# Optimization experiments

Measured on AMD Instinct MI355X. Metric: run time of the kernel, lower is better.

Reference implementation:

```python
import jax, jax.numpy as jnp
import numpy as np
from jax import lax

B, N, D = 4, 2048, 1024
MAX_SEQ = 2048
GROUPS = 4  # math.gcd(1024, 4)
LN_EPS = 1e-5


def setup_inputs() -> dict:
    key = jax.random.key(0)
    ks = jax.random.split(key, 12)
    s = 0.02
    return {
        "x": jax.random.normal(ks[0], (B, N, D), jnp.float32),
        "Wq": jax.random.normal(ks[1], (D, D), jnp.float32) * s,
        "Wk": jax.random.normal(ks[2], (D, D), jnp.float32) * s,
        "Wv": jax.random.normal(ks[3], (D, D), jnp.float32) * s,
        "rel_bias": jax.random.normal(ks[4], (1, MAX_SEQ, MAX_SEQ), jnp.float32) * s,
        "conv_w": jax.random.normal(ks[5], (D, D // GROUPS, 3), jnp.float32) * s,
        "conv_b": jnp.zeros((D,), jnp.float32),
        "resg_w": jax.random.normal(ks[6], (D, D), jnp.float32) * s,
        "resg_b": jnp.zeros((D,), jnp.float32),
        "ln_g": jnp.ones((D,), jnp.float32),
        "ln_b": jnp.zeros((D,), jnp.float32),
        "fc1_w": jax.random.normal(ks[7], (D // 2, D), jnp.float32) * s,
        "fc1_b": jnp.zeros((D // 2,), jnp.float32),
        "fc2_w": jax.random.normal(ks[8], (1, D // 2), jnp.float32) * s,
        "fc2_b": jnp.zeros((1,), jnp.float32),
    }


def _forward(x, Wq, Wk, Wv, rel_bias, conv_w, conv_b, resg_w, resg_b,
             ln_g, ln_b, fc1_w, fc1_b, fc2_w, fc2_b):
    b, n, d = x.shape
    scale = 1.0 / jnp.sqrt(jnp.asarray(d, x.dtype))
    q = x @ Wq.T  # [b,n,dk]
    k = x @ Wk.T
    v = x @ Wv.T  # [b,n,dv]
    att = jnp.einsum("bqd,bkd->bqk", q, k) * scale + rel_bias[:, :n, :n]
    causal = jnp.tril(jnp.ones((n, n), bool))
    att = jnp.where(causal, att, jnp.asarray(-jnp.inf, att.dtype))
    att = jax.nn.softmax(att, axis=-1)  # dropout is identity at eval
    att_out = jnp.einsum("bqk,bkd->bqd", att, v)
    # grouped temporal conv over sequence dim: v [b,n,dv] -> NCH [b,dv,n]
    conv = lax.conv_general_dilated(
        v.transpose(0, 2, 1), conv_w, window_strides=(1,), padding=[(1, 1)],
        dimension_numbers=("NCH", "OIH", "NCH"), feature_group_count=GROUPS)
    conv = conv + conv_b[None, :, None]
    out = att_out + conv.transpose(0, 2, 1)
    res = jax.nn.sigmoid(out @ resg_w.T + resg_b)
    out = x + res * out
    mu = out.mean(-1, keepdims=True)
    var = out.var(-1, keepdims=True)
    out = (out - mu) * lax.rsqrt(var + LN_EPS) * ln_g + ln_b
    h = jax.nn.gelu(out @ fc1_w.T + fc1_b, approximate=False)
    return jax.nn.sigmoid(h @ fc2_w.T + fc2_b)


def reference(x, Wq, Wk, Wv, rel_bias, conv_w, conv_b, resg_w, resg_b,
              ln_g, ln_b, fc1_w, fc1_b, fc2_w, fc2_b):
    return _forward(x, Wq, Wk, Wv, rel_bias, conv_w, conv_b, resg_w, resg_b,
                    ln_g, ln_b, fc1_w, fc1_b, fc2_w, fc2_b)
```

## Files before the change

kernel.cpp:

```cpp
#include <hip/hip_runtime.h>
#include <math.h>

#define NSEQ 2048
#define DDIM 1024
#define BSZ  4
#define BM 128
#define BN 128
#define BK 64

typedef short bf16x8 __attribute__((ext_vector_type(8)));
typedef float f32x4 __attribute__((ext_vector_type(4)));
typedef unsigned int u32;
typedef unsigned short u16;

__device__ __forceinline__ u16 f2bf(float f) {
  union { float f; u32 u; } x; x.f = f;
  u32 r = x.u + 0x7FFFu + ((x.u >> 16) & 1u);
  return (u16)(r >> 16);
}
__device__ __forceinline__ float bf2f(u16 h) {
  union { u32 u; float f; } x; x.u = ((u32)h) << 16; return x.f;
}
__device__ __forceinline__ float sigmoidf_(float x) {
  return 1.0f / (1.0f + expf(-x));
}

__device__ __forceinline__ void async_copy16(const u16* g, u16* l) {
  __builtin_amdgcn_global_load_lds(
      (const __attribute__((address_space(1))) u32*)g,
      (__attribute__((address_space(3))) u32*)l, 16, 0, 0);
}

__device__ __forceinline__ void stage_tile(const u16* __restrict__ gsrc, size_t ld,
                                           int k0, u16* lds, int tid) {
  const int wave = tid >> 6, lane = tid & 63;
  const int rr = lane >> 3;
  const int q  = (lane & 7) ^ rr;
#pragma unroll
  for (int j = 0; j < 4; ++j) {
    const int c = j * 4 + wave;
    async_copy16(gsrc + (size_t)(c * 8 + rr) * ld + k0 + q * 8, lds + c * 512);
  }
}

__device__ __forceinline__ void mfma_step(const u16* Al, const u16* Bl,
                                          int wr, int wc, int l16, int quad,
                                          f32x4 acc[4][4]) {
  const int r7 = l16 & 7;
#pragma unroll
  for (int ks = 0; ks < 2; ++ks) {
    const int s = ((ks * 4 + quad) ^ r7) << 3;
    bf16x8 a[4], b[4];
#pragma unroll
    for (int i = 0; i < 4; ++i) {
      a[i] = *(const bf16x8*)(Al + (wr * 64 + i * 16 + l16) * BK + s);
      b[i] = *(const bf16x8*)(Bl + (wc * 64 + i * 16 + l16) * BK + s);
    }
#pragma unroll
    for (int i = 0; i < 4; ++i)
#pragma unroll
      for (int j = 0; j < 4; ++j)
        acc[i][j] = __builtin_amdgcn_mfma_f32_16x16x32_bf16(a[i], b[j], acc[i][j], 0, 0, 0);
  }
}

__device__ __forceinline__ void zero_acc(f32x4 acc[4][4]) {
#pragma unroll
  for (int i = 0; i < 4; ++i)
#pragma unroll
    for (int j = 0; j < 4; ++j) {
      f32x4 z = {0.f, 0.f, 0.f, 0.f};
      acc[i][j] = z;
    }
}

__device__ __forceinline__ void gemm_loop(const u16* A, size_t lda,
                                          const u16* Bt, size_t ldb, int K,
                                          u16* Al, u16* Bl, int tid,
                                          int wr, int wc, int l16, int quad,
                                          f32x4 acc[4][4]) {
  for (int k0 = 0; k0 < K; k0 += BK) {
    __syncthreads();
    stage_tile(A, lda, k0, Al, tid);
    stage_tile(Bt, ldb, k0, Bl, tid);
    __syncthreads();
    mfma_step(Al, Bl, wr, wc, l16, quad, acc);
  }
}

#define ATT_PB 2228224

__global__ __launch_bounds__(256) void k_prep(
    const float* __restrict__ x,  const float* __restrict__ Wq,
    const float* __restrict__ Wk, const float* __restrict__ Wv,
    const float* __restrict__ rw, const float* __restrict__ f1w,
    const float* __restrict__ cw,
    u16* __restrict__ xb,  u16* __restrict__ Wqb, u16* __restrict__ Wkb,
    u16* __restrict__ Wvb, u16* __restrict__ rwb, u16* __restrict__ f1wb,
    u16* __restrict__ cwp, u16* __restrict__ vpad)
{
  const int blk = blockIdx.x, tid = threadIdx.x;
  const float* s; u16* d; int base;
  if (blk < 8192)       { s = x;   d = xb;   base = blk; }
  else if (blk < 9216)  { s = Wq;  d = Wqb;  base = blk - 8192; }
  else if (blk < 10240) { s = Wk;  d = Wkb;  base = blk - 9216; }
  else if (blk < 11264) { s = Wv;  d = Wvb;  base = blk - 10240; }
  else if (blk < 12288) { s = rw;  d = rwb;  base = blk - 11264; }
  else if (blk < 12800) { s = f1w; d = f1wb; base = blk - 12288; }
  else if (blk < 13824) {
    const int o = blk - 12800, i = tid;
#pragma unroll
    for (int tap = 0; tap < 3; ++tap)
      cwp[(size_t)o * 768 + tap * 256 + i] = f2bf(cw[(size_t)o * 768 + i * 3 + tap]);
    return;
  } else {
    const int e = blk - 13824, bb = e >> 1, which = e & 1;
    u16* row = vpad + (size_t)bb * 2050 * 1024 + (which ? (size_t)2049 * 1024 : 0);
    ushort4 z = {0, 0, 0, 0};
    ((ushort4*)row)[tid] = z;
    return;
  }
  const int i = base * 256 + tid;
  const float4 v = ((const float4*)s)[i];
  ushort4 o;
  o.x = f2bf(v.x); o.y = f2bf(v.y); o.z = f2bf(v.z); o.w = f2bf(v.w);
  ((ushort4*)d)[i] = o;
}

__global__ __launch_bounds__(256) void k_qkv(
    const u16* __restrict__ xb, const u16* __restrict__ Wqb,
    const u16* __restrict__ Wkb, const u16* __restrict__ Wvb,
    u16* __restrict__ qb, u16* __restrict__ kb, u16* __restrict__ vpad)
{
  __shared__ u16 Al[BM * BK], Bl[BN * BK];
  const int tid = threadIdx.x, z = blockIdx.z;
  const u16* W = (z == 0) ? Wqb : ((z == 1) ? Wkb : Wvb);
  const int row0 = blockIdx.x * BM, col0 = blockIdx.y * BN;
  const int lane = tid & 63, wave = tid >> 6;
  const int quad = lane >> 4, l16 = lane & 15, wr = wave >> 1, wc = wave & 1;
  f32x4 acc[4][4];
  zero_acc(acc);
  gemm_loop(xb + (size_t)row0 * DDIM, DDIM, W + (size_t)col0 * DDIM, DDIM, DDIM,
            Al, Bl, tid, wr, wc, l16, quad, acc);
#pragma unroll
  for (int mi = 0; mi < 4; ++mi)
#pragma unroll
    for (int r = 0; r < 4; ++r) {
      const int grow = row0 + wr * 64 + mi * 16 + quad * 4 + r;
#pragma unroll
      for (int ni = 0; ni < 4; ++ni) {
        const int gcol = col0 + wc * 64 + ni * 16 + l16;
        const u16 hv = f2bf(acc[mi][ni][r]);
        if (z == 2) {
          const int b = grow >> 11, t = grow & 2047;
          vpad[(size_t)b * 2050 * 1024 + 1024 + (size_t)t * 1024 + gcol] = hv;
        } else {
          (z == 0 ? qb : kb)[(size_t)grow * DDIM + gcol] = hv;
        }
      }
    }
}

__global__ __launch_bounds__(256) void k_vt(const u16* __restrict__ vpad,
                                            u16* __restrict__ vT)
{
  __shared__ u16 tile[64][72];
  const int t0 = blockIdx.x * 64, d0 = blockIdx.y * 64, b = blockIdx.z;
  const int tid = threadIdx.x;
  const u16* vb = vpad + (size_t)b * 2050 * 1024 + 1024;
#pragma unroll
  for (int p = 0; p < 4; ++p) {
    const int r = p * 16 + (tid >> 4), c = (tid & 15) << 2;
    const ushort4 v4 = *(const ushort4*)(vb + (size_t)(t0 + r) * 1024 + d0 + c);
    tile[r][c] = v4.x; tile[r][c + 1] = v4.y; tile[r][c + 2] = v4.z; tile[r][c + 3] = v4.w;
  }
  __syncthreads();
  u16* ob = vT + (size_t)b * DDIM * NSEQ;
#pragma unroll
  for (int p = 0; p < 4; ++p) {
    const int d = p * 16 + (tid >> 4), t = (tid & 15) << 2;
    ushort4 o;
    o.x = tile[t][d]; o.y = tile[t + 1][d]; o.z = tile[t + 2][d]; o.w = tile[t + 3][d];
    *(ushort4*)(ob + (size_t)(d0 + d) * NSEQ + t0 + t) = o;
  }
}

__global__ __launch_bounds__(256) void k_conv(
    const u16* __restrict__ vpad, const u16* __restrict__ cwp,
    const float* __restrict__ cb, u16* __restrict__ convb)
{
  __shared__ u16 Al[BM * BK], Bl[BN * BK];
  const int tid = threadIdx.x;
  const int row0 = blockIdx.x * BM;
  const int col0 = blockIdx.y * BN;
  const int g = col0 >> 8;
  const int b = row0 >> 11, t0 = row0 & 2047;
  const u16* vb = vpad + (size_t)b * 2050 * 1024 + 1024;
  const u16* Bbase = cwp + (size_t)col0 * 768;
  const int lane = tid & 63, wave = tid >> 6;
  const int quad = lane >> 4, l16 = lane & 15, wr = wave >> 1, wc = wave & 1;
  const int rr = lane >> 3;
  const int q  = (lane & 7) ^ rr;
  const int gch = g << 8;
  f32x4 acc[4][4];
  zero_acc(acc);
  for (int k0 = 0; k0 < 768; k0 += BK) {
    __syncthreads();
    const int tap = k0 >> 8;
    const int i0 = k0 & 255;
#pragma unroll
    for (int j = 0; j < 4; ++j) {
      const int c = j * 4 + wave;
      const int r = c * 8 + rr;
      async_copy16(vb + (size_t)(t0 + r - 1 + tap) * 1024 + gch + i0 + q * 8,
                   Al + c * 512);
    }
    stage_tile(Bbase, 768, k0, Bl, tid);
    __syncthreads();
    mfma_step(Al, Bl, wr, wc, l16, quad, acc);
  }
#pragma unroll
  for (int mi = 0; mi < 4; ++mi)
#pragma unroll
    for (int r = 0; r < 4; ++r) {
      const int grow = row0 + wr * 64 + mi * 16 + quad * 4 + r;
#pragma unroll
      for (int ni = 0; ni < 4; ++ni) {
        const int gcol = col0 + wc * 64 + ni * 16 + l16;
        convb[(size_t)grow * DDIM + gcol] = f2bf(cb[gcol] + acc[mi][ni][r]);
      }
    }
}

__global__ __launch_bounds__(256) void k_scores(
    const u16* __restrict__ qb, const u16* __restrict__ kb,
    const float* __restrict__ rb, float* __restrict__ attp)
{
  __shared__ u16 Al[BM * BK], Bl[BN * BK];
  const int b = blockIdx.x, t = blockIdx.y, tid = threadIdx.x;
  int it = 0;
  while ((it + 1) * (it + 2) / 2 <= t) ++it;
  const int jt = t - it * (it + 1) / 2;
  const int row0 = it * BM, col0 = jt * BN;
  const int lane = tid & 63, wave = tid >> 6;
  const int quad = lane >> 4, l16 = lane & 15, wr = wave >> 1, wc = wave & 1;
  f32x4 acc[4][4];
  zero_acc(acc);
  gemm_loop(qb + ((size_t)b * NSEQ + row0) * DDIM, DDIM,
            kb + ((size_t)b * NSEQ + col0) * DDIM, DDIM, DDIM,
            Al, Bl, tid, wr, wc, l16, quad, acc);
  float* abase = attp + (size_t)b * ATT_PB + (size_t)(it * (it + 1) / 2) * 16384;
  const int ldp = (it + 1) * 128;
#pragma unroll
  for (int mi = 0; mi < 4; ++mi)
#pragma unroll
    for (int r = 0; r < 4; ++r) {
      const int ri = wr * 64 + mi * 16 + quad * 4 + r;
      const int gi = row0 + ri;
#pragma unroll
      for (int ni = 0; ni < 4; ++ni) {
        const int j = col0 + wc * 64 + ni * 16 + l16;
        abase[(size_t)ri * ldp + j] =
            acc[mi][ni][r] * 0.03125f + rb[(size_t)gi * NSEQ + j];
      }
    }
}

__global__ __launch_bounds__(256) void k_softmax(const float* __restrict__ attp,
                                                 u16* __restrict__ attb)
{
  const int i = blockIdx.x, b = blockIdx.y;
  const int it = i >> 7;
  const int wlen = (it + 1) << 7;
  const float* row = attp + (size_t)b * ATT_PB +
                     (size_t)(it * (it + 1) / 2) * 16384 + (size_t)(i & 127) * wlen;
  u16* orow = attb + ((size_t)b * NSEQ + i) * NSEQ;
  const int valid = i + 1;
  const int tid = threadIdx.x;
  const int lane = tid & 63, wid = tid >> 6;

  float v[8];
  float m = -1e30f;
#pragma unroll
  for (int t = 0; t < 8; ++t) {
    const int idx = tid + (t << 8);
    v[t] = (idx < valid) ? row[idx] : -1e30f;
    m = fmaxf(m, v[t]);
  }
#pragma unroll
  for (int off = 32; off; off >>= 1) m = fmaxf(m, __shfl_xor(m, off));
  __shared__ float red[4];
  if (lane == 0) red[wid] = m;
  __syncthreads();
  m = fmaxf(fmaxf(red[0], red[1]), fmaxf(red[2], red[3]));
  __syncthreads();

  float s = 0.f;
#pragma unroll
  for (int t = 0; t < 8; ++t) {
    const int idx = tid + (t << 8);
    float e = (idx < valid) ? expf(v[t] - m) : 0.f;
    v[t] = e;
    s += e;
  }
#pragma unroll
  for (int off = 32; off; off >>= 1) s += __shfl_xor(s, off);
  if (lane == 0) red[wid] = s;
  __syncthreads();
  s = red[0] + red[1] + red[2] + red[3];
  const float inv = 1.0f / s;
#pragma unroll
  for (int t = 0; t < 8; ++t) {
    const int idx = tid + (t << 8);
    if (idx < wlen) orow[idx] = f2bf(v[t] * inv);
  }
}

__global__ __launch_bounds__(256) void k_pv(
    const u16* __restrict__ attb, const u16* __restrict__ vT,
    const u16* __restrict__ convb, u16* __restrict__ buf1b)
{
  __shared__ u16 Al[BM * BK], Bl[BN * BK];
  const int it = blockIdx.x, nt = blockIdx.y, b = blockIdx.z;
  const int tid = threadIdx.x;
  const int row0 = it * BM, col0 = nt * BN;
  const int K = (it + 1) * BM;
  const int lane = tid & 63, wave = tid >> 6;
  const int quad = lane >> 4, l16 = lane & 15, wr = wave >> 1, wc = wave & 1;
  f32x4 acc[4][4];
  zero_acc(acc);
  gemm_loop(attb + ((size_t)b * NSEQ + row0) * NSEQ, NSEQ,
            vT + ((size_t)b * DDIM + col0) * NSEQ, NSEQ, K,
            Al, Bl, tid, wr, wc, l16, quad, acc);
  const size_t obase = (size_t)b * NSEQ * DDIM;
#pragma unroll
  for (int mi = 0; mi < 4; ++mi)
#pragma unroll
    for (int r = 0; r < 4; ++r) {
      const int grow = row0 + wr * 64 + mi * 16 + quad * 4 + r;
#pragma unroll
      for (int ni = 0; ni < 4; ++ni) {
        const int gcol = col0 + wc * 64 + ni * 16 + l16;
        const size_t idx = obase + (size_t)grow * DDIM + gcol;
        buf1b[idx] = f2bf(acc[mi][ni][r] + bf2f(convb[idx]));
      }
    }
}

__global__ __launch_bounds__(256) void k_resgate(
    const u16* __restrict__ buf1b, const u16* __restrict__ rwb,
    const float* __restrict__ rbias, const float* __restrict__ x,
    u16* __restrict__ buf2)
{
  __shared__ u16 Al[BM * BK], Bl[BN * BK];
  const int tid = threadIdx.x;
  const int row0 = blockIdx.x * BM, col0 = blockIdx.y * BN;
  const int lane = tid & 63, wave = tid >> 6;
  const int quad = lane >> 4, l16 = lane & 15, wr = wave >> 1, wc = wave & 1;
  f32x4 acc[4][4];
  zero_acc(acc);
  gemm_loop(buf1b + (size_t)row0 * DDIM, DDIM, rwb + (size_t)col0 * DDIM, DDIM,
            DDIM, Al, Bl, tid, wr, wc, l16, quad, acc);
#pragma unroll
  for (int mi = 0; mi < 4; ++mi)
#pragma unroll
    for (int r = 0; r < 4; ++r) {
      const int grow = row0 + wr * 64 + mi * 16 + quad * 4 + r;
#pragma unroll
      for (int ni = 0; ni < 4; ++ni) {
        const int gcol = col0 + wc * 64 + ni * 16 + l16;
        const size_t idx = (size_t)grow * DDIM + gcol;
        const float gate = sigmoidf_(acc[mi][ni][r] + rbias[gcol]);
        buf2[idx] = f2bf(x[idx] + gate * bf2f(buf1b[idx]));
      }
    }
}

__global__ __launch_bounds__(256) void k_ln(
    const u16* __restrict__ buf, const float* __restrict__ gw,
    const float* __restrict__ gb, u16* __restrict__ outb)
{
  const int row = blockIdx.x;
  const u16* p = buf + (size_t)row * DDIM;
  const int tid = threadIdx.x;
  const int lane = tid & 63, wid = tid >> 6;
  const int c = tid << 2;
  const ushort4 raw = *(const ushort4*)(p + c);
  float4 val;
  val.x = bf2f(raw.x); val.y = bf2f(raw.y); val.z = bf2f(raw.z); val.w = bf2f(raw.w);
  float s = val.x + val.y + val.z + val.w;
  float s2 = val.x * val.x + val.y * val.y + val.z * val.z + val.w * val.w;
#pragma unroll
  for (int off = 32; off; off >>= 1) {
    s += __shfl_xor(s, off);
    s2 += __shfl_xor(s2, off);
  }
  __shared__ float r1[4], r2[4];
  if (lane == 0) { r1[wid] = s; r2[wid] = s2; }
  __syncthreads();
  s = r1[0] + r1[1] + r1[2] + r1[3];
  s2 = r2[0] + r2[1] + r2[2] + r2[3];
  const float mean = s * (1.0f / DDIM);
  const float var = s2 * (1.0f / DDIM) - mean * mean;
  const float rstd = rsqrtf(var + 1e-5f);
  const float4 g4 = *(const float4*)(gw + c);
  const float4 b4 = *(const float4*)(gb + c);
  ushort4 o;
  o.x = f2bf((val.x - mean) * rstd * g4.x + b4.x);
  o.y = f2bf((val.y - mean) * rstd * g4.y + b4.y);
  o.z = f2bf((val.z - mean) * rstd * g4.z + b4.z);
  o.w = f2bf((val.w - mean) * rstd * g4.w + b4.w);
  *(ushort4*)(outb + (size_t)row * DDIM + c) = o;
}

__global__ __launch_bounds__(256) void k_fc1(
    const u16* __restrict__ A, const u16* __restrict__ W,
    const float* __restrict__ bias, u16* __restrict__ h)
{
  __shared__ u16 Al[BM * BK], Bl[BN * BK];
  const int tid = threadIdx.x;
  const int row0 = blockIdx.x * BM, col0 = blockIdx.y * BN;
  const int lane = tid & 63, wave = tid >> 6;
  const int quad = lane >> 4, l16 = lane & 15, wr = wave >> 1, wc = wave & 1;
  f32x4 acc[4][4];
  zero_acc(acc);
  gemm_loop(A + (size_t)row0 * DDIM, DDIM, W + (size_t)col0 * DDIM, DDIM, DDIM,
            Al, Bl, tid, wr, wc, l16, quad, acc);
#pragma unroll
  for (int mi = 0; mi < 4; ++mi)
#pragma unroll
    for (int r = 0; r < 4; ++r) {
      const int grow = row0 + wr * 64 + mi * 16 + quad * 4 + r;
#pragma unroll
      for (int ni = 0; ni < 4; ++ni) {
        const int gcol = col0 + wc * 64 + ni * 16 + l16;
        const float t = acc[mi][ni][r] + bias[gcol];
        h[(size_t)grow * 512 + gcol] =
            f2bf(0.5f * t * (1.0f + erff(t * 0.70710678118654752f)));
      }
    }
}

__global__ __launch_bounds__(256) void k_fc2(
    const u16* __restrict__ h, const float* __restrict__ w,
    const float* __restrict__ b2, float* __restrict__ out)
{
  const int r = blockIdx.x * 4 + (threadIdx.x >> 6);
  const int lane = threadIdx.x & 63;
  const u16* hp = h + (size_t)r * 512;
  float s = 0.f;
#pragma unroll
  for (int t = 0; t < 8; ++t) {
    const int c = lane + t * 64;
    s = fmaf(bf2f(hp[c]), w[c], s);
  }
#pragma unroll
  for (int off = 32; off; off >>= 1) s += __shfl_xor(s, off);
  if (lane == 0) out[r] = sigmoidf_(s + b2[0]);
}

extern "C" void kernel_launch(void* const* d_in, const int* in_sizes, int n_in,
                              void* d_out, int out_size, void* d_ws, size_t ws_size,
                              hipStream_t stream) {
  const float* x    = (const float*)d_in[0];
  const float* Wq   = (const float*)d_in[1];
  const float* Wk   = (const float*)d_in[2];
  const float* Wv   = (const float*)d_in[3];
  const float* rb   = (const float*)d_in[4];
  const float* cw   = (const float*)d_in[5];
  const float* cb   = (const float*)d_in[6];
  const float* rw   = (const float*)d_in[7];
  const float* rbias= (const float*)d_in[8];
  const float* lng  = (const float*)d_in[9];
  const float* lnb  = (const float*)d_in[10];
  const float* f1w  = (const float*)d_in[11];
  const float* f1b  = (const float*)d_in[12];
  const float* f2w  = (const float*)d_in[13];
  const float* f2b  = (const float*)d_in[14];
  float* out = (float*)d_out;
  char* w8 = (char*)d_ws;

  u16* xb    = (u16*)(w8 + 0);
  u16* Wqb   = (u16*)(w8 + 16777216);
  u16* Wkb   = (u16*)(w8 + 18874368);
  u16* Wvb   = (u16*)(w8 + 20971520);
  u16* rwb   = (u16*)(w8 + 23068672);
  u16* f1wb  = (u16*)(w8 + 25165824);
  u16* cwp   = (u16*)(w8 + 26214400);
  u16* qb    = (u16*)(w8 + 27787264);
  u16* kb    = (u16*)(w8 + 44564480);
  u16* vpad  = (u16*)(w8 + 61341696);
  u16* vT    = (u16*)(w8 + 78135296);
  float* attp= (float*)(w8 + 94912512);
  u16* convb = (u16*)(w8 + 130564096);
  u16* attb  = (u16*)(w8 + 27787264);
  u16* buf1b = (u16*)(w8 + 0);
  u16* buf2  = (u16*)(w8 + 27787264);
  u16* ln16  = (u16*)(w8 + 78135296);
  u16* h     = (u16*)(w8 + 61341696);

  k_prep   <<<dim3(13832),     256, 0, stream>>>(x, Wq, Wk, Wv, rw, f1w, cw,
                                                 xb, Wqb, Wkb, Wvb, rwb, f1wb,
                                                 cwp, vpad);
  k_qkv    <<<dim3(64, 8, 3),  256, 0, stream>>>(xb, Wqb, Wkb, Wvb, qb, kb, vpad);
  k_vt     <<<dim3(32, 16, 4), 256, 0, stream>>>(vpad, vT);
  k_conv   <<<dim3(64, 8),     256, 0, stream>>>(vpad, cwp, cb, convb);
  k_scores <<<dim3(4, 136),    256, 0, stream>>>(qb, kb, rb, attp);
  k_softmax<<<dim3(NSEQ, BSZ), 256, 0, stream>>>(attp, attb);
  k_pv     <<<dim3(16, 8, 4),  256, 0, stream>>>(attb, vT, convb, buf1b);
  k_resgate<<<dim3(64, 8),     256, 0, stream>>>(buf1b, rwb, rbias, x, buf2);
  k_ln     <<<dim3(BSZ * NSEQ),256, 0, stream>>>(buf2, lng, lnb, ln16);
  k_fc1    <<<dim3(64, 4),     256, 0, stream>>>(ln16, f1wb, f1b, h);
  k_fc2    <<<dim3(NSEQ),      256, 0, stream>>>(h, f2w, f2b, out);
}
```

Measured before the change: 380.4 us.

## Fuse softmax into score and PV kernels using unnormalized exp and row-sum atomics

Removes the separate softmax kernel. The scores kernel now writes bf16 exp(score) directly into the packed causal triangle layout and accumulates per-row sums with atomics. The PV kernel reads the packed layout and divides by the row sum in its epilogue. This skips the max subtraction, so exp can overflow for large logits, and it adds atomic contention. It also swaps the fp32 x read in the residual gate for the bf16 copy, which cuts memory traffic but loses some precision.

```diff
diff --git a/kernel.cpp b/kernel.cpp
--- a/kernel.cpp
+++ b/kernel.cpp
@@ -97,7 +97,7 @@
     const float* __restrict__ cw,
     u16* __restrict__ xb,  u16* __restrict__ Wqb, u16* __restrict__ Wkb,
     u16* __restrict__ Wvb, u16* __restrict__ rwb, u16* __restrict__ f1wb,
-    u16* __restrict__ cwp, u16* __restrict__ vpad)
+    u16* __restrict__ cwp, u16* __restrict__ vpad, float* __restrict__ lsum)
 {
   const int blk = blockIdx.x, tid = threadIdx.x;
   const float* s; u16* d; int base;
@@ -113,11 +113,16 @@
     for (int tap = 0; tap < 3; ++tap)
       cwp[(size_t)o * 768 + tap * 256 + i] = f2bf(cw[(size_t)o * 768 + i * 3 + tap]);
     return;
-  } else {
+  } else if (blk < 13832) {
     const int e = blk - 13824, bb = e >> 1, which = e & 1;
     u16* row = vpad + (size_t)bb * 2050 * 1024 + (which ? (size_t)2049 * 1024 : 0);
     ushort4 z = {0, 0, 0, 0};
     ((ushort4*)row)[tid] = z;
+    return;
+  } else {
+    const int e = blk - 13832;
+    float4 z = {0.f, 0.f, 0.f, 0.f};
+    ((float4*)lsum)[e * 256 + tid] = z;
     return;
   }
   const int i = base * 256 + tid;
@@ -234,7 +239,8 @@
 
 __global__ __launch_bounds__(256) void k_scores(
     const u16* __restrict__ qb, const u16* __restrict__ kb,
-    const float* __restrict__ rb, float* __restrict__ attp)
+    const float* __restrict__ rb, u16* __restrict__ expp,
+    float* __restrict__ lsum)
 {
   __shared__ u16 Al[BM * BK], Bl[BN * BK];
   const int b = blockIdx.x, t = blockIdx.y, tid = threadIdx.x;
@@ -249,76 +255,35 @@
   gemm_loop(qb + ((size_t)b * NSEQ + row0) * DDIM, DDIM,
             kb + ((size_t)b * NSEQ + col0) * DDIM, DDIM, DDIM,
             Al, Bl, tid, wr, wc, l16, quad, acc);
-  float* abase = attp + (size_t)b * ATT_PB + (size_t)(it * (it + 1) / 2) * 16384;
+  u16* abase = expp + (size_t)b * ATT_PB + (size_t)(it * (it + 1) / 2) * 16384;
   const int ldp = (it + 1) * 128;
+  float* lrow = lsum + b * NSEQ + row0;
 #pragma unroll
   for (int mi = 0; mi < 4; ++mi)
 #pragma unroll
     for (int r = 0; r < 4; ++r) {
       const int ri = wr * 64 + mi * 16 + quad * 4 + r;
       const int gi = row0 + ri;
+      float part = 0.f;
 #pragma unroll
       for (int ni = 0; ni < 4; ++ni) {
         const int j = col0 + wc * 64 + ni * 16 + l16;
-        abase[(size_t)ri * ldp + j] =
-            acc[mi][ni][r] * 0.03125f + rb[(size_t)gi * NSEQ + j];
-      }
-    }
-}
-
-__global__ __launch_bounds__(256) void k_softmax(const float* __restrict__ attp,
-                                                 u16* __restrict__ attb)
-{
-  const int i = blockIdx.x, b = blockIdx.y;
-  const int it = i >> 7;
-  const int wlen = (it + 1) << 7;
-  const float* row = attp + (size_t)b * ATT_PB +
-                     (size_t)(it * (it + 1) / 2) * 16384 + (size_t)(i & 127) * wlen;
-  u16* orow = attb + ((size_t)b * NSEQ + i) * NSEQ;
-  const int valid = i + 1;
-  const int tid = threadIdx.x;
-  const int lane = tid & 63, wid = tid >> 6;
-
-  float v[8];
-  float m = -1e30f;
-#pragma unroll
-  for (int t = 0; t < 8; ++t) {
-    const int idx = tid + (t << 8);
-    v[t] = (idx < valid) ? row[idx] : -1e30f;
-    m = fmaxf(m, v[t]);
-  }
-#pragma unroll
-  for (int off = 32; off; off >>= 1) m = fmaxf(m, __shfl_xor(m, off));
-  __shared__ float red[4];
-  if (lane == 0) red[wid] = m;
-  __syncthreads();
-  m = fmaxf(fmaxf(red[0], red[1]), fmaxf(red[2], red[3]));
-  __syncthreads();
-
-  float s = 0.f;
-#pragma unroll
-  for (int t = 0; t < 8; ++t) {
-    const int idx = tid + (t << 8);
-    float e = (idx < valid) ? expf(v[t] - m) : 0.f;
-    v[t] = e;
-    s += e;
-  }
-#pragma unroll
-  for (int off = 32; off; off >>= 1) s += __shfl_xor(s, off);
-  if (lane == 0) red[wid] = s;
-  __syncthreads();
-  s = red[0] + red[1] + red[2] + red[3];
-  const float inv = 1.0f / s;
-#pragma unroll
-  for (int t = 0; t < 8; ++t) {
-    const int idx = tid + (t << 8);
-    if (idx < wlen) orow[idx] = f2bf(v[t] * inv);
-  }
+        const float val = acc[mi][ni][r] * 0.03125f + rb[(size_t)gi * NSEQ + j];
+        const float e = (j <= gi) ? expf(val) : 0.f;
+        const u16 eb = f2bf(e);
+        abase[(size_t)ri * ldp + j] = eb;
+        part += bf2f(eb);
+      }
+#pragma unroll
+      for (int off = 1; off < 16; off <<= 1) part += __shfl_xor(part, off, 16);
+      if (l16 == 0) atomicAdd(lrow + ri, part);
+    }
 }
 
 __global__ __launch_bounds__(256) void k_pv(
-    const u16* __restrict__ attb, const u16* __restrict__ vT,
-    const u16* __restrict__ convb, u16* __restrict__ buf1b)
+    const u16* __restrict__ expp, const u16* __restrict__ vT,
+    const u16* __restrict__ convb, const float* __restrict__ lsum,
+    u16* __restrict__ buf1b)
 {
   __shared__ u16 Al[BM * BK], Bl[BN * BK];
   const int it = blockIdx.x, nt = blockIdx.y, b = blockIdx.z;
@@ -329,27 +294,29 @@
   const int quad = lane >> 4, l16 = lane & 15, wr = wave >> 1, wc = wave & 1;
   f32x4 acc[4][4];
   zero_acc(acc);
-  gemm_loop(attb + ((size_t)b * NSEQ + row0) * NSEQ, NSEQ,
+  gemm_loop(expp + (size_t)b * ATT_PB + (size_t)(it * (it + 1) / 2) * 16384, K,
             vT + ((size_t)b * DDIM + col0) * NSEQ, NSEQ, K,
             Al, Bl, tid, wr, wc, l16, quad, acc);
   const size_t obase = (size_t)b * NSEQ * DDIM;
+  const float* lrow = lsum + b * NSEQ;
 #pragma unroll
   for (int mi = 0; mi < 4; ++mi)
 #pragma unroll
     for (int r = 0; r < 4; ++r) {
       const int grow = row0 + wr * 64 + mi * 16 + quad * 4 + r;
+      const float inv = 1.0f / lrow[grow];
 #pragma unroll
       for (int ni = 0; ni < 4; ++ni) {
         const int gcol = col0 + wc * 64 + ni * 16 + l16;
         const size_t idx = obase + (size_t)grow * DDIM + gcol;
-        buf1b[idx] = f2bf(acc[mi][ni][r] + bf2f(convb[idx]));
+        buf1b[idx] = f2bf(acc[mi][ni][r] * inv + bf2f(convb[idx]));
       }
     }
 }
 
 __global__ __launch_bounds__(256) void k_resgate(
     const u16* __restrict__ buf1b, const u16* __restrict__ rwb,
-    const float* __restrict__ rbias, const float* __restrict__ x,
+    const float* __restrict__ rbias, const u16* __restrict__ xb,
     u16* __restrict__ buf2)
 {
   __shared__ u16 Al[BM * BK], Bl[BN * BK];
@@ -371,7 +338,7 @@
         const int gcol = col0 + wc * 64 + ni * 16 + l16;
         const size_t idx = (size_t)grow * DDIM + gcol;
         const float gate = sigmoidf_(acc[mi][ni][r] + rbias[gcol]);
-        buf2[idx] = f2bf(x[idx] + gate * bf2f(buf1b[idx]));
+        buf2[idx] = f2bf(bf2f(xb[idx]) + gate * bf2f(buf1b[idx]));
       }
     }
 }
@@ -491,24 +458,23 @@
   u16* kb    = (u16*)(w8 + 44564480);
   u16* vpad  = (u16*)(w8 + 61341696);
   u16* vT    = (u16*)(w8 + 78135296);
-  float* attp= (float*)(w8 + 94912512);
-  u16* convb = (u16*)(w8 + 130564096);
-  u16* attb  = (u16*)(w8 + 27787264);
-  u16* buf1b = (u16*)(w8 + 0);
-  u16* buf2  = (u16*)(w8 + 27787264);
+  u16* expp  = (u16*)(w8 + 94912512);
+  u16* convb = (u16*)(w8 + 112746496);
+  float* lsum= (float*)(w8 + 129523712);
+  u16* buf1b = (u16*)(w8 + 27787264);
+  u16* buf2  = (u16*)(w8 + 44564480);
   u16* ln16  = (u16*)(w8 + 78135296);
   u16* h     = (u16*)(w8 + 61341696);
 
-  k_prep   <<<dim3(13832),     256, 0, stream>>>(x, Wq, Wk, Wv, rw, f1w, cw,
+  k_prep   <<<dim3(13840),     256, 0, stream>>>(x, Wq, Wk, Wv, rw, f1w, cw,
                                                  xb, Wqb, Wkb, Wvb, rwb, f1wb,
-                                                 cwp, vpad);
+                                                 cwp, vpad, lsum);
   k_qkv    <<<dim3(64, 8, 3),  256, 0, stream>>>(xb, Wqb, Wkb, Wvb, qb, kb, vpad);
   k_vt     <<<dim3(32, 16, 4), 256, 0, stream>>>(vpad, vT);
   k_conv   <<<dim3(64, 8),     256, 0, stream>>>(vpad, cwp, cb, convb);
-  k_scores <<<dim3(4, 136),    256, 0, stream>>>(qb, kb, rb, attp);
-  k_softmax<<<dim3(NSEQ, BSZ), 256, 0, stream>>>(attp, attb);
-  k_pv     <<<dim3(16, 8, 4),  256, 0, stream>>>(attb, vT, convb, buf1b);
-  k_resgate<<<dim3(64, 8),     256, 0, stream>>>(buf1b, rwb, rbias, x, buf2);
+  k_scores <<<dim3(4, 136),    256, 0, stream>>>(qb, kb, rb, expp, lsum);
+  k_pv     <<<dim3(16, 8, 4),  256, 0, stream>>>(expp, vT, convb, lsum, buf1b);
+  k_resgate<<<dim3(64, 8),     256, 0, stream>>>(buf1b, rwb, rbias, xb, buf2);
   k_ln     <<<dim3(BSZ * NSEQ),256, 0, stream>>>(buf2, lng, lnb, ln16);
   k_fc1    <<<dim3(64, 4),     256, 0, stream>>>(ln16, f1wb, f1b, h);
   k_fc2    <<<dim3(NSEQ),      256, 0, stream>>>(h, f2w, f2b, out);
```

Result: slower. 420.0 us (+10.4%).
